# Kernel tuning notes

Measured on AMD Instinct MI355X. Metric: run time of the kernel, lower is better.

## Reference

```python
import jax, jax.numpy as jnp
import numpy as np

CH = 64
CF = CH // 8  # f/g projection channels


def setup_inputs() -> dict:
    key = jax.random.key(0)
    k1, k2, k3, k4, k5 = jax.random.split(key, 5)
    x = jax.random.normal(k1, (8, 64, 64, CH), dtype=jnp.float32)
    kernel_f = 0.02 * jax.random.normal(k2, (1, 1, CH, CF), dtype=jnp.float32)
    kernel_g = 0.02 * jax.random.normal(k3, (1, 1, CH, CF), dtype=jnp.float32)
    kernel_h = 0.02 * jax.random.normal(k4, (1, 1, CH, CH), dtype=jnp.float32)
    gamma = 0.02 * jax.random.normal(k5, (1,), dtype=jnp.float32)
    return {"x": x, "kernel_f": kernel_f, "kernel_g": kernel_g,
            "kernel_h": kernel_h, "gamma": gamma}


def reference(x, kernel_f, kernel_g, kernel_h, gamma):
    B, H, W, C = x.shape
    N = H * W
    xf = x.reshape(B, N, C)  # flatten spatial; 1x1 conv == matmul over channels
    f = jnp.einsum('bnc,cd->bnd', xf, kernel_f[0, 0])  # [B,N,CF]
    g = jnp.einsum('bnc,cd->bnd', xf, kernel_g[0, 0])  # [B,N,CF]
    h = jnp.einsum('bnc,cd->bnd', xf, kernel_h[0, 0])  # [B,N,C]
    s = jnp.einsum('bnd,bmd->bnm', g, f)  # g @ f^T, [B,N,N]
    beta = jax.nn.softmax(s, axis=-1)
    o = jnp.einsum('bnm,bmc->bnc', beta, h)  # [B,N,C]
    out = gamma * o.reshape(B, H, W, C) + x
    return out
```

## Files before the change

### kernel.cpp

```cpp
#include <hip/hip_runtime.h>
#include <hip/hip_bf16.h>

typedef __attribute__((ext_vector_type(4)))  float f32x4;
typedef __attribute__((ext_vector_type(16))) float f32x16;
typedef __attribute__((ext_vector_type(8)))  short bf16x8;

#define LOG2E 1.44269504088896340736f

#if __has_builtin(__builtin_amdgcn_exp2f)
static __device__ __forceinline__ float exp2_native(float x) {
  return __builtin_amdgcn_exp2f(x);
}
#else
extern "C" __device__ float __ocml_native_exp2_f32(float);
static __device__ __forceinline__ float exp2_native(float x) {
  return __ocml_native_exp2_f32(x);
}
#endif

static __device__ __forceinline__ unsigned int pack_trunc_f(float a, float b) {
  return __builtin_amdgcn_perm(__float_as_uint(b), __float_as_uint(a), 0x07060302);
}

typedef const __attribute__((address_space(1))) unsigned int gu32;
typedef __attribute__((address_space(3))) unsigned int lu32;
static __device__ __forceinline__ void gload_lds16(const void* g, void* l) {
  __builtin_amdgcn_global_load_lds((gu32*)g, (lu32*)l, 16, 0, 0);
}

__global__ __launch_bounds__(256) void proj_kernel(
    const float* __restrict__ x, const float* __restrict__ kf,
    const float* __restrict__ kg, const float* __restrict__ kh,
    unsigned short* __restrict__ f_b, unsigned short* __restrict__ g_b,
    unsigned short* __restrict__ h_p)
{
  __shared__ unsigned short Kt[80*72];
  const int t = threadIdx.x, blk = blockIdx.x;

  #pragma unroll
  for (int r = 0; r < 20; ++r) {
    int idx = r*256 + t;
    int o = idx >> 6, c = idx & 63;
    float v = (o < 8) ? kf[c*8 + o]
            : (o < 16) ? kg[c*8 + (o-8)] * LOG2E
            : kh[c*64 + (o-16)];
    Kt[o*72 + c] = (unsigned short)(__float_as_uint(v) >> 16);
  }
  __syncthreads();

  const int w = t >> 6, lane = t & 63, l15 = lane & 15, quad = lane >> 4;
  const int Rbase = blk*64 + w*16;
  const int R = Rbase + l15;

  bf16x8 af[2];
  #pragma unroll
  for (int kk = 0; kk < 2; ++kk) {
    const float* xp = x + (long)R*64 + kk*32 + quad*8;
    float4 v0 = *(const float4*)xp;
    float4 v1 = *(const float4*)(xp + 4);
    union { unsigned int u[4]; bf16x8 v; } p;
    p.u[0] = pack_trunc_f(v0.x, v0.y);
    p.u[1] = pack_trunc_f(v0.z, v0.w);
    p.u[2] = pack_trunc_f(v1.x, v1.y);
    p.u[3] = pack_trunc_f(v1.z, v1.w);
    af[kk] = p.v;
  }

  f32x4 acc[5];
  #pragma unroll
  for (int nt = 0; nt < 5; ++nt) { f32x4 z = {}; acc[nt] = z; }

  #pragma unroll
  for (int nt = 0; nt < 5; ++nt)
    #pragma unroll
    for (int kk = 0; kk < 2; ++kk) {
      bf16x8 bfv = *(const bf16x8*)&Kt[(nt*16 + l15)*72 + kk*32 + quad*8];
      acc[nt] = __builtin_amdgcn_mfma_f32_16x16x32_bf16(af[kk], bfv, acc[nt], 0, 0, 0);
    }

  const int bt = Rbase >> 12;
  const int kt = (Rbase >> 7) & 31;
  const int base = ((blk & 1) << 6) + (w << 4);
  const int pi = base + ((quad & 1) << 3) + (((quad >> 1) & 1) << 2);

  #pragma unroll
  for (int rr = 0; rr < 4; ++rr) {
    const int nq = (Rbase + quad*4 + rr) & 4095;
    unsigned short v = (unsigned short)(__float_as_uint(acc[0][rr]) >> 16);
    if (l15 < 8) f_b[((long)bt*4096 + nq)*8 + l15] = v;
    else         g_b[((long)bt*4096 + nq)*8 + (l15 - 8)] = v;
  }
  #pragma unroll
  for (int nt = 1; nt < 5; ++nt) {
    const int c = (nt - 1)*16 + l15;
    uint2 v;
    v.x = pack_trunc_f(acc[nt][0], acc[nt][1]);
    v.y = pack_trunc_f(acc[nt][2], acc[nt][3]);
    *(uint2*)(h_p + ((long)(bt*32 + kt)*64 + c)*136 + pi) = v;
  }
}

__global__ __launch_bounds__(256) void attn_kernel(
    const unsigned short* __restrict__ f_b, const unsigned short* __restrict__ g_b,
    const unsigned short* __restrict__ h_p,
    const float* __restrict__ x, const float* __restrict__ gamma_p,
    float* __restrict__ out)
{
  __shared__ unsigned short bufs[2][9728];

  const int t = threadIdx.x;
  const int w = t >> 6, lane = t & 63, l31 = lane & 31, a = lane >> 5;
  const int qb = blockIdx.x, b = blockIdx.y;
  const int q0w = qb*128 + w*32;

  bf16x8 gfv;
  {
    bf16x8 gv = *(const bf16x8*)(g_b + ((long)b*4096 + q0w + l31)*8);
    bf16x8 z = {};
    gfv = (a == 0) ? gv : z;
  }

  f32x16 oacc[2];
  { f32x16 z = {}; oacc[0] = z; oacc[1] = z; }
  float l_run = 0.f;

  const char* hp_b = (const char*)h_p + (long)b*32*17408;
  const char* fb_b = (const char*)f_b + (long)b*4096*16;

  auto stage = [&](int bi, int kt) {
    const char* hsrc = hp_b + (long)kt*17408;
    const char* fsrc = fb_b + (long)kt*2048;
    char* dst = (char*)&bufs[bi][0];
    #pragma unroll
    for (int i = 0; i < 5; ++i) {
      const int off = i*4096 + w*1024;
      if (off < 19456) {
        const char* src = (off < 17408) ? (hsrc + off) : (fsrc + (off - 17408));
        gload_lds16(src + lane*16, dst + off);
      }
    }
  };

  stage(0, 0);

  for (int ktl = 0; ktl < 32; ++ktl) {
    __syncthreads();
    if (ktl < 31) stage((ktl + 1) & 1, ktl + 1);

    const unsigned short* hts = &bufs[ktl & 1][0];
    const unsigned short* fts = &bufs[ktl & 1][8704];

    #pragma unroll
    for (int mt = 0; mt < 4; ++mt) {
      bf16x8 afv = *(const bf16x8*)&fts[(mt*32 + l31)*8];
      f32x16 zz = {};
      f32x16 sc = __builtin_amdgcn_mfma_f32_32x32x16_bf16(afv, gfv, zz, 0, 0, 0);

      #pragma unroll
      for (int half = 0; half < 2; ++half) {
        const int s = mt*2 + half;
        bf16x8 bh0 = *(const bf16x8*)&hts[(l31)*136      + s*16 + a*8];
        bf16x8 bh1 = *(const bf16x8*)&hts[(32 + l31)*136 + s*16 + a*8];
        union { unsigned int u[4]; bf16x8 v; } ap;
        #pragma unroll
        for (int j = 0; j < 4; ++j) {
          float ea = exp2_native(sc[half*8 + 2*j]);
          float eb = exp2_native(sc[half*8 + 2*j + 1]);
          l_run += ea;
          l_run += eb;
          ap.u[j] = pack_trunc_f(ea, eb);
        }
        oacc[0] = __builtin_amdgcn_mfma_f32_32x32x16_bf16(ap.v, bh0, oacc[0], 0, 0, 0);
        oacc[1] = __builtin_amdgcn_mfma_f32_32x32x16_bf16(ap.v, bh1, oacc[1], 0, 0, 0);
      }
    }
  }

  const float l = l_run + __shfl_xor(l_run, 32);
  const float gamma = gamma_p[0];
  const float* xb = x + ((long)b*4096 + q0w)*64;
  float* ob = out + ((long)b*4096 + q0w)*64;

  #pragma unroll
  for (int r = 0; r < 16; ++r) {
    const int q = (r & 3) + 8*(r >> 2) + 4*a;
    const float lq = __shfl(l, q);
    const float s = gamma / lq;
    #pragma unroll
    for (int nt = 0; nt < 2; ++nt) {
      const long idx = (long)q*64 + nt*32 + l31;
      ob[idx] = fmaf(s, oacc[nt][r], xb[idx]);
    }
  }
}

extern "C" void kernel_launch(void* const* d_in, const int* in_sizes, int n_in,
                              void* d_out, int out_size, void* d_ws, size_t ws_size,
                              hipStream_t stream) {
  const float* x  = (const float*)d_in[0];
  const float* kf = (const float*)d_in[1];
  const float* kg = (const float*)d_in[2];
  const float* kh = (const float*)d_in[3];
  const float* gamma = (const float*)d_in[4];
  float* out = (float*)d_out;

  char* ws = (char*)d_ws;
  unsigned short* h_p = (unsigned short*)ws;
  unsigned short* f_b = (unsigned short*)(ws + 4456448);
  unsigned short* g_b = (unsigned short*)(ws + 4980736);

  proj_kernel<<<512, 256, 0, stream>>>(x, kf, kg, kh, f_b, g_b, h_p);
  attn_kernel<<<dim3(32, 8), 256, 0, stream>>>(f_b, g_b, h_p, x, gamma, out);
}
```

Baseline: 116.1 us.

## Split attention key range across warp pairs and compute row sums via MFMA

The attention kernel now uses 64 queries per block instead of 128. Two warp groups each process half of the key tiles, which doubles the grid to 512 blocks so the GPU's compute units are better filled. Partial outputs are combined through shared memory at the end. The softmax denominator is now produced by an extra MFMA against a ones vector, replacing the scalar per-lane accumulation. The cost is a larger dynamic LDS footprint (76 KB), one more MFMA per step, a cross-warp reduction, and each block loading its own f/h tiles, which doubles total tile traffic.

```diff
diff --git a/kernel.cpp b/kernel.cpp
--- a/kernel.cpp
+++ b/kernel.cpp
@@ -100,18 +100,19 @@
   }
 }
 
-__global__ __launch_bounds__(256) void attn_kernel(
+__global__ __launch_bounds__(256, 2) void attn_kernel(
     const unsigned short* __restrict__ f_b, const unsigned short* __restrict__ g_b,
     const unsigned short* __restrict__ h_p,
     const float* __restrict__ x, const float* __restrict__ gamma_p,
     float* __restrict__ out)
 {
-  __shared__ unsigned short bufs[2][9728];
+  extern __shared__ char smem[];
 
   const int t = threadIdx.x;
   const int w = t >> 6, lane = t & 63, l31 = lane & 31, a = lane >> 5;
+  const int qg = w & 1, kh = w >> 1;
   const int qb = blockIdx.x, b = blockIdx.y;
-  const int q0w = qb*128 + w*32;
+  const int q0w = qb*64 + qg*32;
 
   bf16x8 gfv;
   {
@@ -119,22 +120,32 @@
     bf16x8 z = {};
     gfv = (a == 0) ? gv : z;
   }
-
-  f32x16 oacc[2];
-  { f32x16 z = {}; oacc[0] = z; oacc[1] = z; }
-  float l_run = 0.f;
+  bf16x8 bhl;
+  {
+    union { unsigned short s[8]; bf16x8 v; } o8;
+    #pragma unroll
+    for (int j = 0; j < 8; ++j) o8.s[j] = 0x3F80;
+    bf16x8 z = {};
+    bhl = (l31 == 0) ? o8.v : z;
+  }
+
+  f32x16 oacc[2], ol;
+  { f32x16 z = {}; oacc[0] = z; oacc[1] = z; ol = z; }
 
   const char* hp_b = (const char*)h_p + (long)b*32*17408;
   const char* fb_b = (const char*)f_b + (long)b*4096*16;
-
-  auto stage = [&](int bi, int kt) {
+  char* sbase = smem + kh*38912;
+
+  auto stage = [&](int bi, int ktl) {
+    const int kt = kh*16 + ktl;
     const char* hsrc = hp_b + (long)kt*17408;
     const char* fsrc = fb_b + (long)kt*2048;
-    char* dst = (char*)&bufs[bi][0];
-    #pragma unroll
-    for (int i = 0; i < 5; ++i) {
-      const int off = i*4096 + w*1024;
-      if (off < 19456) {
+    char* dst = sbase + bi*19456;
+    #pragma unroll
+    for (int i = 0; i < 10; ++i) {
+      const int c = i*2 + qg;
+      if (c < 19) {
+        const int off = c*1024;
         const char* src = (off < 17408) ? (hsrc + off) : (fsrc + (off - 17408));
         gload_lds16(src + lane*16, dst + off);
       }
@@ -143,12 +154,12 @@
 
   stage(0, 0);
 
-  for (int ktl = 0; ktl < 32; ++ktl) {
+  for (int ktl = 0; ktl < 16; ++ktl) {
     __syncthreads();
-    if (ktl < 31) stage((ktl + 1) & 1, ktl + 1);
-
-    const unsigned short* hts = &bufs[ktl & 1][0];
-    const unsigned short* fts = &bufs[ktl & 1][8704];
+    if (ktl < 15) stage((ktl + 1) & 1, ktl + 1);
+
+    const unsigned short* hts = (const unsigned short*)(sbase + (ktl & 1)*19456);
+    const unsigned short* fts = hts + 8704;
 
     #pragma unroll
     for (int mt = 0; mt < 4; ++mt) {
@@ -166,30 +177,46 @@
         for (int j = 0; j < 4; ++j) {
           float ea = exp2_native(sc[half*8 + 2*j]);
           float eb = exp2_native(sc[half*8 + 2*j + 1]);
-          l_run += ea;
-          l_run += eb;
           ap.u[j] = pack_trunc_f(ea, eb);
         }
         oacc[0] = __builtin_amdgcn_mfma_f32_32x32x16_bf16(ap.v, bh0, oacc[0], 0, 0, 0);
         oacc[1] = __builtin_amdgcn_mfma_f32_32x32x16_bf16(ap.v, bh1, oacc[1], 0, 0, 0);
+        ol      = __builtin_amdgcn_mfma_f32_32x32x16_bf16(ap.v, bhl, ol,      0, 0, 0);
       }
     }
   }
 
-  const float l = l_run + __shfl_xor(l_run, 32);
-  const float gamma = gamma_p[0];
-  const float* xb = x + ((long)b*4096 + q0w)*64;
-  float* ob = out + ((long)b*4096 + q0w)*64;
-
-  #pragma unroll
-  for (int r = 0; r < 16; ++r) {
-    const int q = (r & 3) + 8*(r >> 2) + 4*a;
-    const float lq = __shfl(l, q);
-    const float s = gamma / lq;
-    #pragma unroll
-    for (int nt = 0; nt < 2; ++nt) {
-      const long idx = (long)q*64 + nt*32 + l31;
-      ob[idx] = fmaf(s, oacc[nt][r], xb[idx]);
+  __syncthreads();
+  float* cb = (float*)smem;
+  if (kh == 1) {
+    float* d = cb + (qg*64 + lane)*48;
+    #pragma unroll
+    for (int r = 0; r < 16; ++r) {
+      d[r] = oacc[0][r]; d[16 + r] = oacc[1][r]; d[32 + r] = ol[r];
+    }
+  }
+  __syncthreads();
+  if (kh == 0) {
+    const float* sp = cb + (qg*64 + lane)*48;
+    #pragma unroll
+    for (int r = 0; r < 16; ++r) {
+      oacc[0][r] += sp[r]; oacc[1][r] += sp[16 + r]; ol[r] += sp[32 + r];
+    }
+
+    const float gamma = gamma_p[0];
+    const float* xb = x + ((long)b*4096 + q0w)*64;
+    float* ob = out + ((long)b*4096 + q0w)*64;
+
+    #pragma unroll
+    for (int r = 0; r < 16; ++r) {
+      const int q = (r & 3) + 8*(r >> 2) + 4*a;
+      const float lq = __shfl(ol[r], lane & 32);
+      const float s = gamma / lq;
+      #pragma unroll
+      for (int nt = 0; nt < 2; ++nt) {
+        const long idx = (long)q*64 + nt*32 + l31;
+        ob[idx] = fmaf(s, oacc[nt][r], xb[idx]);
+      }
     }
   }
 }
@@ -210,5 +237,5 @@
   unsigned short* g_b = (unsigned short*)(ws + 4980736);
 
   proj_kernel<<<512, 256, 0, stream>>>(x, kf, kg, kh, f_b, g_b, h_p);
-  attn_kernel<<<dim3(32, 8), 256, 0, stream>>>(f_b, g_b, h_p, x, gamma, out);
-}
+  attn_kernel<<<dim3(64, 8), 256, 77824, stream>>>(f_b, g_b, h_p, x, gamma, out);
+}
```

New measurement: 109.3 us. 1.06x faster.
